# Kernel tuning notes

Hardware: AMD Instinct MI355X
Metric: run time of the kernel (lower is better)

The kernel has to match this reference:

```python
import jax, jax.numpy as jnp
import numpy as np

B, S, D = 8, 2048, 1024

def setup_inputs() -> dict:
    key = jax.random.key(0)
    ks = jax.random.split(key, 7)
    s = 1.0 / np.sqrt(D)
    return {
        "x": jax.random.normal(ks[0], (B, S, D), dtype=jnp.float32),
        "Wq": jax.random.normal(ks[1], (D, D), dtype=jnp.float32) * s,
        "bq": jnp.zeros((D,), dtype=jnp.float32),
        "Wk": jax.random.normal(ks[2], (D, D), dtype=jnp.float32) * s,
        "bk": jnp.zeros((D,), dtype=jnp.float32),
        "Wv": jax.random.normal(ks[3], (D, D), dtype=jnp.float32) * s,
        "bv": jnp.zeros((D,), dtype=jnp.float32),
    }

def reference(x, Wq, bq, Wk, bk, Wv, bv):
    # QKV projections: [B,S,D]
    q = x @ Wq + bq
    k = x @ Wk + bk
    v = x @ Wv + bv
    # scores scaled by sqrt(full input_dim) — single head, per source
    scores = jnp.einsum("bsd,btd->bst", q, k) / jnp.sqrt(jnp.float32(D))
    attn = jax.nn.softmax(scores, axis=2)
    return jnp.einsum("bst,btd->bsd", attn, v)
```

## Files before the change

### kernel.cpp

```cpp
#include <hip/hip_runtime.h>

typedef _Float16 half8 __attribute__((ext_vector_type(8)));
typedef float floatx4 __attribute__((ext_vector_type(4)));

#define AS1 __attribute__((address_space(1)))
#define AS3 __attribute__((address_space(3)))

__global__ __launch_bounds__(256) void wtrans_kernel(
    const float* __restrict__ W0, const float* __restrict__ W1,
    const float* __restrict__ W2, _Float16* __restrict__ Wt)
{
    __shared__ _Float16 t[64 * 72];
    const float* W = (blockIdx.z == 0) ? W0 : (blockIdx.z == 1) ? W1 : W2;
    _Float16* O = Wt + (long)blockIdx.z * 1048576;
    const int tid = threadIdx.x;
    const int kb = blockIdx.y * 64, nb = blockIdx.x * 64;
#pragma unroll
    for (int i = 0; i < 4; i++) {
        int r = (tid >> 4) + i * 16;
        int c = (tid & 15) * 4;
        floatx4 w = *(const floatx4*)&W[(long)(kb + r) * 1024 + nb + c];
#pragma unroll
        for (int j = 0; j < 4; j++) t[(c + j) * 72 + r] = (_Float16)w[j];
    }
    __syncthreads();
    const int c = tid >> 2, rch = (tid & 3) * 16;
    half8 v0 = *(const half8*)&t[c * 72 + rch];
    half8 v1 = *(const half8*)&t[c * 72 + rch + 8];
    _Float16* o = &O[(long)(nb + c) * 1024 + kb + rch];
    *(half8*)o = v0;
    *(half8*)(o + 8) = v1;
}

__global__ __launch_bounds__(256) void f32_to_f16_kernel(
    const float* __restrict__ in, _Float16* __restrict__ out, int n)
{
    for (long i = ((long)blockIdx.x * 256 + threadIdx.x) * 8; i < n;
         i += (long)gridDim.x * 256 * 8) {
        floatx4 a = *(const floatx4*)&in[i];
        floatx4 b = *(const floatx4*)&in[i + 4];
        half8 h;
#pragma unroll
        for (int e = 0; e < 4; e++) { h[e] = (_Float16)a[e]; h[e + 4] = (_Float16)b[e]; }
        *(half8*)&out[i] = h;
    }
}

template <int MODE>
__global__ __launch_bounds__(256) void gemm128_kernel(
    const _Float16* __restrict__ A, const _Float16* __restrict__ Bt,
    void* __restrict__ Cv, const float* __restrict__ bias,
    const float* __restrict__ bias2,
    int nx, int ny,
    int K, int lda, int ldb, int ldc,
    long aBatch, long bBatch, long cBatch, float scale)
{
    constexpr int SMEM_ELEMS = (MODE == 1) ? 17408 : 16384;
    __shared__ _Float16 smem[SMEM_ELEMS];
    _Float16* Ash = smem;
    _Float16* Bsh = smem + 8192;

    const int tid = threadIdx.x;
    const int wave = tid >> 6, lane = tid & 63;
    const int quad = lane >> 4, lr = lane & 15;
    const int wm = wave & 1, wn = wave >> 1;

    const int P = gridDim.x >> 3;
    const int g = (blockIdx.x & 7) * P + (blockIdx.x >> 3);
    const int pplane = nx * ny;
    const int z = g / pplane;
    const int rr = g - z * pplane;
    const int by = rr / nx;
    const int bx = rr - by * nx;
    const int m0 = by * 128, n0 = bx * 128;

    const _Float16* Ab = A + (long)z * aBatch;
    const _Float16* Bb = Bt + (long)z * bBatch;

    const int srow = tid >> 2;
    const int scol = (tid & 3) * 8;
    const long ag0 = (long)(m0 + srow) * lda + scol;
    const long bg0 = (long)(n0 + srow) * ldb + scol;
    const int sdst = tid * 8;

    floatx4 acc[4][4] = {};

    for (int k0 = 0; k0 < K; k0 += 64) {
#pragma unroll
        for (int s = 0; s < 2; s++) {
            const int kk = k0 + s * 32;
            const int so = s * 4096;
            __builtin_amdgcn_global_load_lds(
                (AS1 void*)(Ab + ag0 + kk), (AS3 void*)(Ash + so + sdst), 16, 0, 0);
            __builtin_amdgcn_global_load_lds(
                (AS1 void*)(Ab + ag0 + (long)64 * lda + kk), (AS3 void*)(Ash + so + sdst + 2048), 16, 0, 0);
            __builtin_amdgcn_global_load_lds(
                (AS1 void*)(Bb + bg0 + kk), (AS3 void*)(Bsh + so + sdst), 16, 0, 0);
            __builtin_amdgcn_global_load_lds(
                (AS1 void*)(Bb + bg0 + (long)64 * ldb + kk), (AS3 void*)(Bsh + so + sdst + 2048), 16, 0, 0);
        }
        __syncthreads();

#pragma unroll
        for (int s = 0; s < 2; s++) {
            const int so = s * 4096;
            half8 aF[4], bF[4];
#pragma unroll
            for (int i = 0; i < 4; i++) {
                aF[i] = *(const half8*)&Ash[so + (wm * 64 + i * 16 + lr) * 32 + quad * 8];
                bF[i] = *(const half8*)&Bsh[so + (wn * 64 + i * 16 + lr) * 32 + quad * 8];
            }
#pragma unroll
            for (int mi = 0; mi < 4; mi++)
#pragma unroll
                for (int ni = 0; ni < 4; ni++)
                    acc[mi][ni] = __builtin_amdgcn_mfma_f32_16x16x32_f16(
                        aF[mi], bF[ni], acc[mi][ni], 0, 0, 0);
        }
        __syncthreads();
    }

    if constexpr (MODE == 0) {
        _Float16* C = (_Float16*)Cv + (long)z * cBatch;
        const float* bz = (z == 0 || !bias2) ? bias : bias2;
#pragma unroll
        for (int ni = 0; ni < 4; ni++) {
            const int n = n0 + wn * 64 + ni * 16 + lr;
            const float bv_ = bz ? bz[n] : 0.0f;
#pragma unroll
            for (int mi = 0; mi < 4; mi++) {
                const int mb = m0 + wm * 64 + mi * 16 + quad * 4;
#pragma unroll
                for (int r = 0; r < 4; r++)
                    C[(long)(mb + r) * ldc + n] = (_Float16)((acc[mi][ni][r] + bv_) * scale);
            }
        }
    } else if constexpr (MODE == 1) {
        _Float16* ctile = smem;
#pragma unroll
        for (int ni = 0; ni < 4; ni++) {
            const int nl = wn * 64 + ni * 16 + lr;
            const float bv_ = bias ? bias[n0 + nl] : 0.0f;
#pragma unroll
            for (int mi = 0; mi < 4; mi++) {
                const int ml = wm * 64 + mi * 16 + quad * 4;
#pragma unroll
                for (int r = 0; r < 4; r++)
                    ctile[nl * 136 + ml + r] = (_Float16)((acc[mi][ni][r] + bv_) * scale);
            }
        }
        __syncthreads();
        _Float16* C = (_Float16*)Cv + (long)(m0 >> 11) * cBatch;
        const int t0 = m0 & 2047;
#pragma unroll
        for (int p = 0; p < 8; p++) {
            const int row = p * 16 + (tid >> 4);
            const int seg = (tid & 15) * 8;
            half8 v = *(const half8*)&ctile[row * 136 + seg];
            *(half8*)&C[(long)(n0 + row) * ldc + t0 + seg] = v;
        }
    } else {
        float* C = (float*)Cv + (long)z * cBatch;
#pragma unroll
        for (int ni = 0; ni < 4; ni++) {
            const int n = n0 + wn * 64 + ni * 16 + lr;
#pragma unroll
            for (int mi = 0; mi < 4; mi++) {
                const int mb = m0 + wm * 64 + mi * 16 + quad * 4;
#pragma unroll
                for (int r = 0; r < 4; r++)
                    C[(long)(mb + r) * ldc + n] = acc[mi][ni][r] * scale;
            }
        }
    }
}

#define STAGE_A(d, h, kt) do { \
    __builtin_amdgcn_global_load_lds((AS1 void*)(Ap + (long)((h) * 64) * lda + (long)(kt) * 64), \
        (AS3 void*)(Ash + (d) * 16384 + (h) * 8192 + sdst), 16, 0, 0); \
    __builtin_amdgcn_global_load_lds((AS1 void*)(Ap + (long)((h) * 64 + 128) * lda + (long)(kt) * 64), \
        (AS3 void*)(Ash + (d) * 16384 + (h) * 8192 + 4096 + sdst), 16, 0, 0); \
} while (0)

#define STAGE_B(d, h, kt) do { \
    __builtin_amdgcn_global_load_lds((AS1 void*)(Bp0 + (long)((h) * 32) * ldb + (long)(kt) * 64), \
        (AS3 void*)(Bsh + (d) * 16384 + (h) * 8192 + sdst), 16, 0, 0); \
    __builtin_amdgcn_global_load_lds((AS1 void*)(Bp1 + (long)((h) * 32) * ldb + (long)(kt) * 64), \
        (AS3 void*)(Bsh + (d) * 16384 + (h) * 8192 + 4096 + sdst), 16, 0, 0); \
} while (0)

#define LDA_FRAGS(d, mh) do { \
    _Pragma("unroll") for (int mi_ = 0; mi_ < 4; mi_++) { \
        const _Float16* p_ = &Ash[(d) * 16384 + (mh) * 8192 + (arow + mi_ * 16) * 64]; \
        aF[mi_][0] = *(const half8*)&p_[kq0]; \
        aF[mi_][1] = *(const half8*)&p_[kq1]; \
    } \
} while (0)

#define LDB_FRAGS(d, nh) do { \
    _Pragma("unroll") for (int ni_ = 0; ni_ < 2; ni_++) { \
        const _Float16* p_ = &Bsh[(d) * 16384 + (nh) * 8192 + (brow + ni_ * 16) * 64]; \
        bF[nh][ni_][0] = *(const half8*)&p_[kq0]; \
        bF[nh][ni_][1] = *(const half8*)&p_[kq1]; \
    } \
} while (0)

#define MFMA16(mh, nh) do { \
    __builtin_amdgcn_s_setprio(1); \
    _Pragma("unroll") for (int mi_ = 0; mi_ < 4; mi_++) \
    _Pragma("unroll") for (int ni_ = 0; ni_ < 2; ni_++) { \
        acc[(mh) * 4 + mi_][(nh) * 2 + ni_] = __builtin_amdgcn_mfma_f32_16x16x32_f16( \
            aF[mi_][0], bF[nh][ni_][0], acc[(mh) * 4 + mi_][(nh) * 2 + ni_], 0, 0, 0); \
        acc[(mh) * 4 + mi_][(nh) * 2 + ni_] = __builtin_amdgcn_mfma_f32_16x16x32_f16( \
            aF[mi_][1], bF[nh][ni_][1], acc[(mh) * 4 + mi_][(nh) * 2 + ni_], 0, 0, 0); \
    } \
    __builtin_amdgcn_s_setprio(0); \
} while (0)

#define VMBAR(n) do { \
    asm volatile("s_waitcnt vmcnt(" #n ")" ::: "memory"); \
    __builtin_amdgcn_s_barrier(); \
    asm volatile("" ::: "memory"); \
} while (0)

template <int MODE>
__global__ __launch_bounds__(512, 2) void gemm256_kernel(
    const _Float16* __restrict__ A, const _Float16* __restrict__ Bt,
    void* __restrict__ Cv, const float* __restrict__ bias,
    const float* __restrict__ bias2,
    int nx, int ny, int K, int lda, int ldb, int ldc,
    long aBatch, long bBatch, long cBatch, float scale)
{
    __shared__ _Float16 smem[65536];
    _Float16* Ash = smem;
    _Float16* Bsh = smem + 32768;

    const int tid = threadIdx.x;
    const int wave = tid >> 6, lane = tid & 63;
    const int quad = lane >> 4, lr = lane & 15;
    const int wm = wave >> 2, wn = wave & 3;

    const int P = gridDim.x >> 3;
    const int g = (blockIdx.x & 7) * P + (blockIdx.x >> 3);
    const int pplane = nx * ny;
    const int z = g / pplane;
    const int rr = g - z * pplane;
    const int by = rr / nx;
    const int bx = rr - by * nx;
    const int m0 = by * 256, n0 = bx * 256;

    const _Float16* Ab = A + (long)z * aBatch;
    const _Float16* Bb = Bt + (long)z * bBatch;

    const int sr0 = tid >> 3;
    const int sc0 = (tid & 7) ^ (sr0 & 7);
    const _Float16* Ap = Ab + (long)(m0 + sr0) * lda + sc0 * 8;
    const int bc0 = (sr0 & 31) + ((sr0 >> 5) << 6);
    const int bc1 = (sr0 & 31) + (((sr0 >> 5) + 2) << 6);
    const _Float16* Bp0 = Bb + (long)(n0 + bc0) * ldb + sc0 * 8;
    const _Float16* Bp1 = Bb + (long)(n0 + bc1) * ldb + sc0 * 8;
    const int sdst = tid * 8;

    const int kq0 = (quad * 8) ^ ((lr & 7) << 3);
    const int kq1 = (32 + quad * 8) ^ ((lr & 7) << 3);
    const int arow = wm * 64 + lr;
    const int brow = wn * 32 + lr;

    half8 aF[4][2];
    half8 bF[2][2][2];
    floatx4 acc[8][4] = {};
    const int NT = K >> 6;
    const int NI = NT >> 1;

    STAGE_A(0, 0, 0); STAGE_B(0, 0, 0); STAGE_B(0, 1, 0); STAGE_A(0, 1, 0);
    STAGE_A(1, 0, 1); STAGE_B(1, 0, 1);
    asm volatile("s_waitcnt vmcnt(4)" ::: "memory");
    __builtin_amdgcn_s_barrier();
    asm volatile("" ::: "memory");

    for (int i = 0; i < NI - 1; ++i) {
        const int t1 = 2 * i + 1, t2 = 2 * i + 2, t3 = 2 * i + 3;
        LDA_FRAGS(0, 0); LDB_FRAGS(0, 0);
        STAGE_B(1, 1, t1);
        VMBAR(8);
        MFMA16(0, 0);
        LDB_FRAGS(0, 1);
        STAGE_A(1, 1, t1);
        VMBAR(8);
        MFMA16(0, 1);
        LDA_FRAGS(0, 1);
        STAGE_A(0, 0, t2);
        VMBAR(8);
        MFMA16(1, 1);
        STAGE_B(0, 0, t2);
        VMBAR(8);
        MFMA16(1, 0);
        LDA_FRAGS(1, 0); LDB_FRAGS(1, 0);
        STAGE_B(0, 1, t2);
        VMBAR(8);
        MFMA16(0, 0);
        LDB_FRAGS(1, 1);
        STAGE_A(0, 1, t2);
        VMBAR(8);
        MFMA16(0, 1);
        LDA_FRAGS(1, 1);
        STAGE_A(1, 0, t3);
        VMBAR(8);
        MFMA16(1, 1);
        STAGE_B(1, 0, t3);
        VMBAR(8);
        MFMA16(1, 0);
    }

    {
        const int tl = NT - 1;
        LDA_FRAGS(0, 0); LDB_FRAGS(0, 0);
        STAGE_B(1, 1, tl);
        VMBAR(8);
        MFMA16(0, 0);
        LDB_FRAGS(0, 1);
        STAGE_A(1, 1, tl);
        VMBAR(8);
        MFMA16(0, 1);
        LDA_FRAGS(0, 1);
        VMBAR(8);
        MFMA16(1, 1);
        VMBAR(4);
        MFMA16(1, 0);
        LDA_FRAGS(1, 0); LDB_FRAGS(1, 0);
        VMBAR(2);
        MFMA16(0, 0);
        LDB_FRAGS(1, 1);
        VMBAR(0);
        MFMA16(0, 1);
        LDA_FRAGS(1, 1);
        MFMA16(1, 1);
        MFMA16(1, 0);
    }

    if constexpr (MODE == 0) {
        _Float16* C = (_Float16*)Cv + (long)z * cBatch;
        const float* bz = (z == 0 || !bias2) ? bias : bias2;
#pragma unroll
        for (int ni = 0; ni < 4; ni++) {
            const int n = n0 + wn * 64 + ni * 16 + lr;
            const float bv_ = bz ? bz[n] : 0.0f;
#pragma unroll
            for (int mi = 0; mi < 8; mi++) {
                const int mb = m0 + wm * 128 + mi * 16 + quad * 4;
#pragma unroll
                for (int r = 0; r < 4; r++)
                    C[(long)(mb + r) * ldc + n] = (_Float16)((acc[mi][ni][r] + bv_) * scale);
            }
        }
    } else {
        float* C = (float*)Cv + (long)z * cBatch;
#pragma unroll
        for (int ni = 0; ni < 4; ni++) {
            const int n = n0 + wn * 64 + ni * 16 + lr;
#pragma unroll
            for (int mi = 0; mi < 8; mi++) {
                const int mb = m0 + wm * 128 + mi * 16 + quad * 4;
#pragma unroll
                for (int r = 0; r < 4; r++)
                    C[(long)(mb + r) * ldc + n] = acc[mi][ni][r] * scale;
            }
        }
    }
}

#undef STAGE_A
#undef STAGE_B
#undef LDA_FRAGS
#undef LDB_FRAGS
#undef MFMA16
#undef VMBAR

__global__ __launch_bounds__(256) void softmax_kernel(_Float16* __restrict__ buf)
{
    const int lane = threadIdx.x & 63;
    const long row = (long)blockIdx.x * 4 + (threadIdx.x >> 6);
    _Float16* p = buf + row * 2048;

    float f[32];
#pragma unroll
    for (int j = 0; j < 4; j++) {
        half8 v = *(const half8*)&p[lane * 8 + j * 512];
#pragma unroll
        for (int e = 0; e < 8; e++) f[j * 8 + e] = (float)v[e];
    }
    float m = -1e30f;
#pragma unroll
    for (int i = 0; i < 32; i++) m = fmaxf(m, f[i]);
#pragma unroll
    for (int off = 32; off; off >>= 1) m = fmaxf(m, __shfl_xor(m, off, 64));
    float s = 0.0f;
#pragma unroll
    for (int i = 0; i < 32; i++) { f[i] = __expf(f[i] - m); s += f[i]; }
#pragma unroll
    for (int off = 32; off; off >>= 1) s += __shfl_xor(s, off, 64);
    const float inv = 1.0f / s;
#pragma unroll
    for (int j = 0; j < 4; j++) {
        half8 v;
#pragma unroll
        for (int e = 0; e < 8; e++) v[e] = (_Float16)(f[j * 8 + e] * inv);
        *(half8*)&p[lane * 8 + j * 512] = v;
    }
}

extern "C" void kernel_launch(void* const* d_in, const int* in_sizes, int n_in,
                              void* d_out, int out_size, void* d_ws, size_t ws_size,
                              hipStream_t stream)
{
    const float* x  = (const float*)d_in[0];
    const float* Wq = (const float*)d_in[1];
    const float* bq = (const float*)d_in[2];
    const float* Wk = (const float*)d_in[3];
    const float* bk = (const float*)d_in[4];
    const float* Wv = (const float*)d_in[5];
    const float* bv = (const float*)d_in[6];

    if (ws_size < 174063616u) return;

    char* ws = (char*)d_ws;
    _Float16* Q  = (_Float16*)(ws + 0);
    _Float16* Vt = (_Float16*)(ws + 67108864);
    _Float16* Sc = (_Float16*)(ws + 100663296);
    _Float16* Wt = (_Float16*)(ws + 167772160);
    _Float16* xb = Sc;
    _Float16* Kb = Q + 16777216;
    float* out = (float*)d_out;

    wtrans_kernel<<<dim3(16, 16, 3), 256, 0, stream>>>(Wq, Wk, Wv, Wt);
    f32_to_f16_kernel<<<2048, 256, 0, stream>>>(x, xb, 16777216);

    gemm256_kernel<0><<<512, 512, 0, stream>>>(
        xb, Wt, Q, bq, bk, 4, 64, 1024, 1024, 1024, 1024,
        0, 1048576, 16777216, 1.0f);
    gemm128_kernel<1><<<1024, 256, 0, stream>>>(
        xb, Wt + 2097152, Vt, bv, nullptr, 8, 128, 1024, 1024, 1024, 2048,
        0, 0, 2097152, 1.0f);

    gemm256_kernel<0><<<512, 512, 0, stream>>>(
        Q, Kb, Sc, nullptr, nullptr, 8, 8, 1024, 1024, 1024, 2048,
        2097152, 2097152, 4194304, 0.03125f);

    softmax_kernel<<<4096, 256, 0, stream>>>(Sc);

    gemm256_kernel<2><<<256, 512, 0, stream>>>(
        Sc, Vt, out, nullptr, nullptr, 4, 8, 2048, 2048, 2048, 1024,
        4194304, 2097152, 2097152, 1.0f);
}
```

Measured before the change: 423.5 us.

## Rotate B fragment registers to prefetch next tile's B half earlier

Splits the B fragment register file into four named sets (B00, B01, B10, B11). The B half for the next k-tile is now loaded from shared memory during the current iteration, and the order of global->LDS staging and MFMA quadrant steps is reshuffled so LDS fragment reads overlap more with MFMA work. This targets exposed LDS read latency before each MFMA block. It raises register pressure, and the vmcnt counts and barrier placement had to be reworked, which risks a stall or hazard if any count is wrong.

```diff
diff --git a/kernel.cpp b/kernel.cpp
--- a/kernel.cpp
+++ b/kernel.cpp
@@ -197,22 +197,22 @@
     } \
 } while (0)
 
-#define LDB_FRAGS(d, nh) do { \
+#define LDB_SET(DSTB, d, nh) do { \
     _Pragma("unroll") for (int ni_ = 0; ni_ < 2; ni_++) { \
         const _Float16* p_ = &Bsh[(d) * 16384 + (nh) * 8192 + (brow + ni_ * 16) * 64]; \
-        bF[nh][ni_][0] = *(const half8*)&p_[kq0]; \
-        bF[nh][ni_][1] = *(const half8*)&p_[kq1]; \
+        DSTB[ni_][0] = *(const half8*)&p_[kq0]; \
+        DSTB[ni_][1] = *(const half8*)&p_[kq1]; \
     } \
 } while (0)
 
-#define MFMA16(mh, nh) do { \
+#define MFMA16(mh, nh, BSET) do { \
     __builtin_amdgcn_s_setprio(1); \
     _Pragma("unroll") for (int mi_ = 0; mi_ < 4; mi_++) \
     _Pragma("unroll") for (int ni_ = 0; ni_ < 2; ni_++) { \
         acc[(mh) * 4 + mi_][(nh) * 2 + ni_] = __builtin_amdgcn_mfma_f32_16x16x32_f16( \
-            aF[mi_][0], bF[nh][ni_][0], acc[(mh) * 4 + mi_][(nh) * 2 + ni_], 0, 0, 0); \
+            aF[mi_][0], BSET[ni_][0], acc[(mh) * 4 + mi_][(nh) * 2 + ni_], 0, 0, 0); \
         acc[(mh) * 4 + mi_][(nh) * 2 + ni_] = __builtin_amdgcn_mfma_f32_16x16x32_f16( \
-            aF[mi_][1], bF[nh][ni_][1], acc[(mh) * 4 + mi_][(nh) * 2 + ni_], 0, 0, 0); \
+            aF[mi_][1], BSET[ni_][1], acc[(mh) * 4 + mi_][(nh) * 2 + ni_], 0, 0, 0); \
     } \
     __builtin_amdgcn_s_setprio(0); \
 } while (0)
@@ -267,75 +267,79 @@
     const int brow = wn * 32 + lr;
 
     half8 aF[4][2];
-    half8 bF[2][2][2];
+    half8 B00[2][2], B01[2][2], B10[2][2], B11[2][2];
     floatx4 acc[8][4] = {};
     const int NT = K >> 6;
     const int NI = NT >> 1;
 
-    STAGE_A(0, 0, 0); STAGE_B(0, 0, 0); STAGE_B(0, 1, 0); STAGE_A(0, 1, 0);
-    STAGE_A(1, 0, 1); STAGE_B(1, 0, 1);
+    STAGE_B(0, 0, 0); STAGE_A(0, 0, 0); STAGE_B(0, 1, 0); STAGE_A(0, 1, 0);
+    STAGE_B(1, 0, 1); STAGE_A(1, 0, 1);
     asm volatile("s_waitcnt vmcnt(4)" ::: "memory");
     __builtin_amdgcn_s_barrier();
     asm volatile("" ::: "memory");
+    LDB_SET(B00, 0, 0);
 
     for (int i = 0; i < NI - 1; ++i) {
         const int t1 = 2 * i + 1, t2 = 2 * i + 2, t3 = 2 * i + 3;
-        LDA_FRAGS(0, 0); LDB_FRAGS(0, 0);
+        LDA_FRAGS(0, 0);
         STAGE_B(1, 1, t1);
         VMBAR(8);
-        MFMA16(0, 0);
-        LDB_FRAGS(0, 1);
+        MFMA16(0, 0, B00);
+        LDB_SET(B01, 0, 1);
         STAGE_A(1, 1, t1);
         VMBAR(8);
-        MFMA16(0, 1);
+        MFMA16(0, 1, B01);
         LDA_FRAGS(0, 1);
+        STAGE_B(0, 0, t2);
+        VMBAR(8);
+        MFMA16(1, 1, B01);
+        LDB_SET(B10, 1, 0);
         STAGE_A(0, 0, t2);
         VMBAR(8);
-        MFMA16(1, 1);
-        STAGE_B(0, 0, t2);
-        VMBAR(8);
-        MFMA16(1, 0);
-        LDA_FRAGS(1, 0); LDB_FRAGS(1, 0);
+        MFMA16(1, 0, B00);
+        LDA_FRAGS(1, 0);
         STAGE_B(0, 1, t2);
         VMBAR(8);
-        MFMA16(0, 0);
-        LDB_FRAGS(1, 1);
+        MFMA16(0, 0, B10);
+        LDB_SET(B11, 1, 1);
         STAGE_A(0, 1, t2);
         VMBAR(8);
-        MFMA16(0, 1);
+        MFMA16(0, 1, B11);
         LDA_FRAGS(1, 1);
+        STAGE_B(1, 0, t3);
+        VMBAR(8);
+        MFMA16(1, 1, B11);
+        LDB_SET(B00, 0, 0);
         STAGE_A(1, 0, t3);
         VMBAR(8);
-        MFMA16(1, 1);
-        STAGE_B(1, 0, t3);
-        VMBAR(8);
-        MFMA16(1, 0);
+        MFMA16(1, 0, B10);
     }
 
     {
         const int tl = NT - 1;
-        LDA_FRAGS(0, 0); LDB_FRAGS(0, 0);
+        LDA_FRAGS(0, 0);
         STAGE_B(1, 1, tl);
         VMBAR(8);
-        MFMA16(0, 0);
-        LDB_FRAGS(0, 1);
+        MFMA16(0, 0, B00);
+        LDB_SET(B01, 0, 1);
         STAGE_A(1, 1, tl);
         VMBAR(8);
-        MFMA16(0, 1);
+        MFMA16(0, 1, B01);
         LDA_FRAGS(0, 1);
-        VMBAR(8);
-        MFMA16(1, 1);
+        VMBAR(6);
+        MFMA16(1, 1, B01);
+        LDB_SET(B10, 1, 0);
         VMBAR(4);
-        MFMA16(1, 0);
-        LDA_FRAGS(1, 0); LDB_FRAGS(1, 0);
+        MFMA16(1, 0, B00);
+        LDA_FRAGS(1, 0);
         VMBAR(2);
-        MFMA16(0, 0);
-        LDB_FRAGS(1, 1);
+        MFMA16(0, 0, B10);
+        LDB_SET(B11, 1, 1);
         VMBAR(0);
-        MFMA16(0, 1);
+        MFMA16(0, 1, B11);
         LDA_FRAGS(1, 1);
-        MFMA16(1, 1);
-        MFMA16(1, 0);
+        MFMA16(1, 1, B11);
+        MFMA16(1, 0, B10);
     }
 
     if constexpr (MODE == 0) {
@@ -372,7 +376,7 @@
 #undef STAGE_A
 #undef STAGE_B
 #undef LDA_FRAGS
-#undef LDB_FRAGS
+#undef LDB_SET
 #undef MFMA16
 #undef VMBAR
 
```

Measured after the change: 427.3 us. No clear change (+0.9%).
